# Performance work log

Hardware: AMD Instinct MI355X
Metric: run time of the kernel (lower is better)

The kernel has to match this reference:

```python
import jax, jax.numpy as jnp
import numpy as np

B, N, C, H = 2, 2048, 1024, 16
D = C // H
SCALE = D ** -0.5


def setup_inputs() -> dict:
    key = jax.random.key(0)
    ks = jax.random.split(key, 5)
    x = jax.random.normal(ks[0], (B, N, C), dtype=jnp.float32)
    # causal mask, broadcast over batch: True = attend
    attention_mask = jnp.broadcast_to(jnp.tril(jnp.ones((N, N), dtype=bool)), (B, N, N))
    w_qkv = jax.random.normal(ks[1], (3 * C, C), dtype=jnp.float32) * (C ** -0.5)
    b_qkv = jax.random.normal(ks[2], (3 * C,), dtype=jnp.float32) * 0.02
    w_proj = jax.random.normal(ks[3], (C, C), dtype=jnp.float32) * (C ** -0.5)
    b_proj = jax.random.normal(ks[4], (C,), dtype=jnp.float32) * 0.02
    return {"x": x, "attention_mask": attention_mask, "w_qkv": w_qkv,
            "b_qkv": b_qkv, "w_proj": w_proj, "b_proj": b_proj}


def reference(x, attention_mask, w_qkv, b_qkv, w_proj, b_proj):
    b, n, c = x.shape
    qkv = x @ w_qkv.T + b_qkv                      # [B,N,3C]
    qkv = qkv.reshape(b, n, 3, H, D).transpose(2, 0, 3, 1, 4)  # [3,B,H,N,D]
    q, k, v = qkv[0], qkv[1], qkv[2]
    dots = jnp.einsum('bhid,bhjd->bhij', q, k) * SCALE
    mask_value = -jnp.finfo(dots.dtype).max
    dots = jnp.where(attention_mask[:, None, :, :], dots, mask_value)
    attn = jax.nn.softmax(dots.astype(jnp.float32), axis=-1).astype(dots.dtype)
    out = jnp.einsum('bhij,bhjd->bhid', attn, v)   # [B,H,N,D]
    # NOTE: original code reshapes WITHOUT transposing heads back - faithful.
    out = out.reshape(b, n, c)
    return out @ w_proj.T + b_proj
```

## Files before the change

### kernel.cpp

```cpp
#include <hip/hip_runtime.h>
#include <hip/hip_bf16.h>
#include <stdint.h>

#define SL_F 0.18033688011112043f

typedef unsigned short u16;
typedef unsigned int u32;
typedef __attribute__((ext_vector_type(8))) short bf16x8;
typedef __attribute__((ext_vector_type(4))) float f32x4;

__device__ __forceinline__ u16 f2bf(float f) {
    union { float f; u32 u; } v; v.f = f;
    return (u16)((v.u + 0x7fffu + ((v.u >> 16) & 1u)) >> 16);
}
__device__ __forceinline__ u32 pack2bf(float a, float b) {
    union { __hip_bfloat162 h; u32 u; } p;
    p.h = __float22bfloat162_rn(make_float2(a, b));
    return p.u;
}

__device__ __forceinline__ void gl_lds16(const u16* g, u16* l) {
    __builtin_amdgcn_global_load_lds(
        (const __attribute__((address_space(1))) u32*)g,
        (__attribute__((address_space(3))) u32*)l, 16, 0, 0);
}

__global__ __launch_bounds__(256) void convert_k(
    const float* __restrict__ x, const float* __restrict__ w1,
    const float* __restrict__ w2,
    u16* __restrict__ xb, u16* __restrict__ w1b, u16* __restrict__ w2b)
{
    const int t = blockIdx.x * 256 + threadIdx.x;
    const int XA = 524288, XW1 = 393216;
    const float* src; u16* dst; int s;
    if (t < XA)            { src = x;  dst = xb;  s = t; }
    else if (t < XA + XW1) { src = w1; dst = w1b; s = t - XA; }
    else                   { src = w2; dst = w2b; s = t - XA - XW1; }
    const int c = s >> 6;
    const int u = s & 63;
    const int l = (u >> 2) + 16 * (u & 3);
    const int g = c >> 5, kb = c & 31;
    const int row = g * 16 + (l & 15);
    const int k0 = kb * 32 + (l >> 4) * 8;
    const float4 v0 = *(const float4*)&src[(size_t)row * 1024 + k0];
    const float4 v1 = *(const float4*)&src[(size_t)row * 1024 + k0 + 4];
    uint4 o;
    o.x = pack2bf(v0.x, v0.y); o.y = pack2bf(v0.z, v0.w);
    o.z = pack2bf(v1.x, v1.y); o.w = pack2bf(v1.z, v1.w);
    *(uint4*)&dst[((size_t)c * 64 + l) * 8] = o;
}

__global__ __launch_bounds__(256) void qkv_gemm(
    const u16* __restrict__ A, const u16* __restrict__ Bw,
    const float* __restrict__ bias,
    u16* __restrict__ Qb, u16* __restrict__ Kb, u16* __restrict__ VTb)
{
    __shared__ __align__(16) u16 Al[2][8 * 512];
    __shared__ __align__(16) u16 Bl[2][8 * 512];
    const int tid = threadIdx.x;
    const int lane = tid & 63;
    const int w = tid >> 6;
    const int la = lane & 15, qd = lane >> 4;
    const int m0 = blockIdx.y * 128;
    const int n0 = blockIdx.x * 128;
    const int wm = (w >> 1) * 64, wn = (w & 1) * 64;

    const u16* Ag0 = A + ((size_t)((m0 >> 4) + 2 * w) * 32) * 512 + lane * 8;
    const u16* Ag1 = Ag0 + 32 * 512;
    const u16* Bg0 = Bw + ((size_t)((n0 >> 4) + 2 * w) * 32) * 512 + lane * 8;
    const u16* Bg1 = Bg0 + 32 * 512;

    auto stage = [&](int k0, int b) {
        const size_t ko = (size_t)(k0 >> 5) * 512;
        gl_lds16(Ag0 + ko, &Al[b][(2 * w) * 512]);
        gl_lds16(Ag1 + ko, &Al[b][(2 * w + 1) * 512]);
        gl_lds16(Bg0 + ko, &Bl[b][(2 * w) * 512]);
        gl_lds16(Bg1 + ko, &Bl[b][(2 * w + 1) * 512]);
    };

    f32x4 acc[4][4] = {};
    int buf = 0;
    stage(0, 0);

    for (int k0 = 0; k0 < 1024; k0 += 32) {
        __syncthreads();
        if (k0 + 32 < 1024) stage(k0 + 32, buf ^ 1);

        bf16x8 af[4], bfr[4];
#pragma unroll
        for (int i = 0; i < 4; i++)
            af[i] = *(const bf16x8*)&Al[buf][(((unsigned)wm >> 4) + i) * 512 + lane * 8];
#pragma unroll
        for (int j = 0; j < 4; j++)
            bfr[j] = *(const bf16x8*)&Bl[buf][(((unsigned)wn >> 4) + j) * 512 + lane * 8];
#pragma unroll
        for (int i = 0; i < 4; i++)
#pragma unroll
            for (int j = 0; j < 4; j++)
                acc[i][j] = __builtin_amdgcn_mfma_f32_16x16x32_bf16(
                    af[i], bfr[j], acc[i][j], 0, 0, 0);
        buf ^= 1;
    }

    const int b_ = m0 >> 11;
    const int nb = (m0 & 2047) + wm;
#pragma unroll
    for (int j = 0; j < 4; j++) {
        const int colb = n0 + wn + j * 16;
        const int col = colb + la;
        const float bv = bias[col];
        const int t = colb >> 10;
        const int hd = col & 1023, h = hd >> 6, d = hd & 63;
        const int bh = b_ * 16 + h;
        if (t == 0) {
            u16* QB = Qb + ((size_t)bh * 2048 + nb) * 64 + d;
#pragma unroll
            for (int i = 0; i < 4; i++)
#pragma unroll
                for (int r = 0; r < 4; r++)
                    QB[(i * 16 + qd * 4 + r) * 64] =
                        f2bf((acc[i][j][r] + bv) * SL_F);
        } else if (t == 1) {
            u16* KB = Kb + (size_t)bh * 131072
                    + (size_t)((nb >> 4) * 2 + (d >> 5)) * 512 + (d & 31);
#pragma unroll
            for (int i = 0; i < 4; i++)
#pragma unroll
                for (int r = 0; r < 4; r++)
                    KB[i * 1024 + (qd * 4 + r) * 32] = f2bf(acc[i][j][r] + bv);
        } else {
            u16* VB = VTb + (size_t)bh * 131072
                    + (size_t)(d >> 4) * 32768 + (d & 15) * 32;
#pragma unroll
            for (int i = 0; i < 4; i++)
#pragma unroll
                for (int r = 0; r < 4; r++)
                    VB[((nb >> 5) + (i >> 1)) * 512 + (i & 1) * 16 + qd * 4 + r]
                        = f2bf(acc[i][j][r] + bv);
        }
    }
}

__global__ __launch_bounds__(256) void proj_gemm(
    const u16* __restrict__ A, const u16* __restrict__ Bw,
    const float* __restrict__ bias, float* __restrict__ Out)
{
    __shared__ __align__(16) u16 Al[2][16 * 512];
    __shared__ __align__(16) u16 Bl[2][8 * 512];
    const int tid = threadIdx.x;
    const int lane = tid & 63;
    const int w = tid >> 6;
    const int la = lane & 15, qd = lane >> 4;
    const int K = 1024;
    const int m0 = blockIdx.y * 128;
    const int n0 = blockIdx.x * 64;
    const int wm = (w >> 1) * 64, wn = (w & 1) * 32;

    const u16* Ab[4];
#pragma unroll
    for (int t = 0; t < 4; t++) {
        const int ck = 4 * w + t, g = ck >> 1, h = ck & 1;
        Ab[t] = A + (((size_t)(m0 >> 4) + g) * 32 + h) * 512 + lane * 8;
    }
    const u16* Bg = Bw + ((size_t)((n0 >> 4) + w) * 32) * 512 + lane * 8;

    auto stage = [&](int k0, int b) {
#pragma unroll
        for (int t = 0; t < 4; t++)
            gl_lds16(Ab[t] + (size_t)(k0 >> 5) * 512, &Al[b][(4 * w + t) * 512]);
#pragma unroll
        for (int t = 0; t < 2; t++)
            gl_lds16(Bg + (size_t)((k0 >> 5) + t) * 512, &Bl[b][(2 * w + t) * 512]);
    };

    f32x4 acc[4][2] = {};
    int buf = 0;
    stage(0, 0);

    for (int k0 = 0; k0 < K; k0 += 64) {
        __syncthreads();
        if (k0 + 64 < K) stage(k0 + 64, buf ^ 1);

        bf16x8 af[4][2], bfr[2][2];
#pragma unroll
        for (int i = 0; i < 4; i++) {
            const int g = ((unsigned)wm >> 4) + i;
#pragma unroll
            for (int h = 0; h < 2; h++)
                af[i][h] = *(const bf16x8*)&Al[buf][(g * 2 + h) * 512 + lane * 8];
        }
#pragma unroll
        for (int j = 0; j < 2; j++) {
            const int g = ((unsigned)wn >> 4) + j;
#pragma unroll
            for (int h = 0; h < 2; h++)
                bfr[j][h] = *(const bf16x8*)&Bl[buf][(g * 2 + h) * 512 + lane * 8];
        }
#pragma unroll
        for (int i = 0; i < 4; i++)
#pragma unroll
            for (int j = 0; j < 2; j++) {
                f32x4 c = acc[i][j];
                c = __builtin_amdgcn_mfma_f32_16x16x32_bf16(af[i][0], bfr[j][0], c, 0, 0, 0);
                c = __builtin_amdgcn_mfma_f32_16x16x32_bf16(af[i][1], bfr[j][1], c, 0, 0, 0);
                acc[i][j] = c;
            }
        buf ^= 1;
    }

#pragma unroll
    for (int j = 0; j < 2; j++) {
        const int col = n0 + wn + j * 16 + la;
        const float bv = bias[col];
#pragma unroll
        for (int i = 0; i < 4; i++)
#pragma unroll
            for (int r = 0; r < 4; r++) {
                const int row = m0 + wm + i * 16 + qd * 4 + r;
                Out[(size_t)row * 1024 + col] = acc[i][j][r] + bv;
            }
    }
}

__global__ __launch_bounds__(512) void attn_k(
    const u16* __restrict__ Qb, const u16* __restrict__ Kb,
    const u16* __restrict__ VTb, u16* __restrict__ Ob)
{
    __shared__ __align__(16) u16 Kl[2][16 * 512];
    __shared__ __align__(16) u16 Vl[2][16 * 512];
    __shared__ __align__(16) u16 Pl[8][16 * 72];
    const int bh = blockIdx.x & 31;
    const int pairT = blockIdx.x >> 5;
    const int tid = threadIdx.x;
    const int lane = tid & 63;
    const int w = tid >> 6;
    const int la = lane & 15, qd = lane >> 4;

    const int perm = (lane & 15) * 32 + (lane >> 4) * 8;
    const u16* Kbh = Kb + (size_t)bh * 131072 + perm;
    const u16* Vbh = VTb + (size_t)bh * 131072 + perm;
    u16* Pw = &Pl[w][0];

    auto stage = [&](int j0, int b) {
#pragma unroll
        for (int t = 0; t < 2; t++) {
            const int ck = 2 * w + t;
            gl_lds16(Kbh + (size_t)((j0 >> 3) + ck) * 512, &Kl[b][ck * 512]);
            gl_lds16(Vbh + (size_t)((ck >> 2) * 64 + (j0 >> 5) + (ck & 3)) * 512,
                     &Vl[b][ck * 512]);
        }
    };

    int buf = 0;
    stage(0, 0);

    for (int half = 0; half < 2; half++) {
        const int tile = (half == 0) ? pairT : 15 - pairT;
        const int q0 = tile * 128 + w * 16;
        const int jmax = tile * 128;
        const int qrow = q0 + la;

        const u16* Qp = Qb + ((size_t)bh * 2048 + q0 + la) * 64 + qd * 8;
        const bf16x8 qf0 = *(const bf16x8*)Qp;
        const bf16x8 qf1 = *(const bf16x8*)(Qp + 32);

        f32x4 o[4] = {};
        float lsum = 0.f;

        for (int j0 = 0; j0 <= jmax; j0 += 128) {
            __syncthreads();

            const int nj = (j0 + 128 <= jmax) ? (j0 + 128) : ((half == 0) ? 0 : -1);
            if (nj >= 0) stage(nj, buf ^ 1);

            f32x4 s[8];
#pragma unroll
            for (int c = 0; c < 8; c++) {
                f32x4 z = {};
                const bf16x8 kf0 = *(const bf16x8*)&Kl[buf][(c * 2 + 0) * 512 + lane * 8];
                const bf16x8 kf1 = *(const bf16x8*)&Kl[buf][(c * 2 + 1) * 512 + lane * 8];
                z = __builtin_amdgcn_mfma_f32_16x16x32_bf16(kf0, qf0, z, 0, 0, 0);
                z = __builtin_amdgcn_mfma_f32_16x16x32_bf16(kf1, qf1, z, 0, 0, 0);
                s[c] = z;
            }

            if (j0 == jmax) {
#pragma unroll
                for (int c = 0; c < 8; c++)
#pragma unroll
                    for (int r = 0; r < 4; r++) {
                        const int j = j0 + c * 16 + qd * 4 + r;
                        float v = s[c][r];
                        v = (j > qrow) ? -1e30f : v;
                        s[c][r] = __builtin_amdgcn_exp2f(v);
                    }
            } else {
#pragma unroll
                for (int c = 0; c < 8; c++)
#pragma unroll
                    for (int r = 0; r < 4; r++)
                        s[c][r] = __builtin_amdgcn_exp2f(s[c][r]);
            }
#pragma unroll
            for (int c = 0; c < 8; c++)
#pragma unroll
                for (int r = 0; r < 4; r++)
                    lsum += s[c][r];

#pragma unroll
            for (int hh = 0; hh < 2; hh++) {
#pragma unroll
                for (int c = 0; c < 4; c++) {
                    uint2 pw;
                    pw.x = pack2bf(s[hh * 4 + c][0], s[hh * 4 + c][1]);
                    pw.y = pack2bf(s[hh * 4 + c][2], s[hh * 4 + c][3]);
                    *(uint2*)&Pw[la * 72 + c * 16 + qd * 4] = pw;
                }
                const bf16x8 pf0 = *(const bf16x8*)&Pw[la * 72 + qd * 8];
                const bf16x8 pf1 = *(const bf16x8*)&Pw[la * 72 + 32 + qd * 8];
#pragma unroll
                for (int c2 = 0; c2 < 4; c2++) {
                    const bf16x8 vf0 = *(const bf16x8*)&Vl[buf][(c2 * 4 + hh * 2 + 0) * 512 + lane * 8];
                    const bf16x8 vf1 = *(const bf16x8*)&Vl[buf][(c2 * 4 + hh * 2 + 1) * 512 + lane * 8];
                    o[c2] = __builtin_amdgcn_mfma_f32_16x16x32_bf16(pf0, vf0, o[c2], 0, 0, 0);
                    o[c2] = __builtin_amdgcn_mfma_f32_16x16x32_bf16(pf1, vf1, o[c2], 0, 0, 0);
                }
            }
            buf ^= 1;
        }

        lsum += __shfl_xor(lsum, 16, 64);
        lsum += __shfl_xor(lsum, 32, 64);
        float rinv[4];
#pragma unroll
        for (int r = 0; r < 4; r++)
            rinv[r] = 1.0f / __shfl(lsum, qd * 4 + r, 64);

        const int m = bh * 128 + (q0 >> 4);
        u16* Ot = Ob + ((size_t)(m >> 4) * 32) * 512;
        const int mm = m & 15;
#pragma unroll
        for (int c2 = 0; c2 < 4; c2++)
#pragma unroll
            for (int r = 0; r < 4; r++) {
                const int kk5 = (qd * 4 + r) * 2 + (c2 >> 1);
                const int s3 = (c2 * 2 + (la >> 3)) & 3;
                Ot[(size_t)kk5 * 512 + (mm + 16 * s3) * 8 + (la & 7)] =
                    f2bf(o[c2][r] * rinv[r]);
            }
    }
}

extern "C" void kernel_launch(void* const* d_in, const int* in_sizes, int n_in,
                              void* d_out, int out_size, void* d_ws, size_t ws_size,
                              hipStream_t stream)
{
    const float* x     = (const float*)d_in[0];
    const float* wqkv  = (const float*)d_in[2];
    const float* bqkv  = (const float*)d_in[3];
    const float* wproj = (const float*)d_in[4];
    const float* bproj = (const float*)d_in[5];
    float* out = (float*)d_out;

    u16* ws     = (u16*)d_ws;
    u16* xb     = ws;
    u16* wqkvb  = xb + 4096 * 1024;
    u16* wprojb = wqkvb + 3072 * 1024;
    u16* Qb     = wprojb + 1024 * 1024;
    u16* Kb     = Qb + 32 * 2048 * 64;
    u16* VTb    = Kb + 32 * 2048 * 64;
    u16* Ob     = VTb + 32 * 2048 * 64;

    convert_k<<<dim3(4096), dim3(256), 0, stream>>>(
        x, wqkv, wproj, xb, wqkvb, wprojb);

    qkv_gemm<<<dim3(24, 32), dim3(256), 0, stream>>>(
        xb, wqkvb, bqkv, Qb, Kb, VTb);

    attn_k<<<dim3(256), dim3(512), 0, stream>>>(Qb, Kb, VTb, Ob);

    proj_gemm<<<dim3(16, 32), dim3(256), 0, stream>>>(
        Ob, wprojb, bproj, out);
}
```

Baseline: 188.4 us.

## Process two 16-row query tiles per wave in attention, halving block size

Each wave in the attention kernel now handles 32 query rows as two 16-row sub-tiles, with 4 waves per block instead of 8. Each K and V fragment read from LDS feeds two MFMAs, which halves LDS read traffic per unit of compute. Each wave also issues twice the staging loads. The cost is roughly double the accumulator and score registers per wave, with launch_bounds(256,1), and only 4 waves per block to hide latency.

```diff
diff --git a/kernel.cpp b/kernel.cpp
--- a/kernel.cpp
+++ b/kernel.cpp
@@ -222,13 +222,13 @@
     }
 }
 
-__global__ __launch_bounds__(512) void attn_k(
+__global__ __launch_bounds__(256, 1) void attn_k(
     const u16* __restrict__ Qb, const u16* __restrict__ Kb,
     const u16* __restrict__ VTb, u16* __restrict__ Ob)
 {
     __shared__ __align__(16) u16 Kl[2][16 * 512];
     __shared__ __align__(16) u16 Vl[2][16 * 512];
-    __shared__ __align__(16) u16 Pl[8][16 * 72];
+    __shared__ __align__(16) u16 Pl[4][2][16 * 72];
     const int bh = blockIdx.x & 31;
     const int pairT = blockIdx.x >> 5;
     const int tid = threadIdx.x;
@@ -239,12 +239,13 @@
     const int perm = (lane & 15) * 32 + (lane >> 4) * 8;
     const u16* Kbh = Kb + (size_t)bh * 131072 + perm;
     const u16* Vbh = VTb + (size_t)bh * 131072 + perm;
-    u16* Pw = &Pl[w][0];
+    u16* PwA = &Pl[w][0][0];
+    u16* PwB = &Pl[w][1][0];
 
     auto stage = [&](int j0, int b) {
 #pragma unroll
-        for (int t = 0; t < 2; t++) {
-            const int ck = 2 * w + t;
+        for (int t = 0; t < 4; t++) {
+            const int ck = 4 * w + t;
             gl_lds16(Kbh + (size_t)((j0 >> 3) + ck) * 512, &Kl[b][ck * 512]);
             gl_lds16(Vbh + (size_t)((ck >> 2) * 64 + (j0 >> 5) + (ck & 3)) * 512,
                      &Vl[b][ck * 512]);
@@ -256,16 +257,19 @@
 
     for (int half = 0; half < 2; half++) {
         const int tile = (half == 0) ? pairT : 15 - pairT;
-        const int q0 = tile * 128 + w * 16;
+        const int q0 = tile * 128 + w * 32;
         const int jmax = tile * 128;
-        const int qrow = q0 + la;
+        const int qrowA = q0 + la;
+        const int qrowB = q0 + 16 + la;
 
         const u16* Qp = Qb + ((size_t)bh * 2048 + q0 + la) * 64 + qd * 8;
-        const bf16x8 qf0 = *(const bf16x8*)Qp;
-        const bf16x8 qf1 = *(const bf16x8*)(Qp + 32);
-
-        f32x4 o[4] = {};
-        float lsum = 0.f;
+        const bf16x8 qfA0 = *(const bf16x8*)Qp;
+        const bf16x8 qfA1 = *(const bf16x8*)(Qp + 32);
+        const bf16x8 qfB0 = *(const bf16x8*)(Qp + 16 * 64);
+        const bf16x8 qfB1 = *(const bf16x8*)(Qp + 16 * 64 + 32);
+
+        f32x4 oA[4] = {}, oB[4] = {};
+        float lsumA = 0.f, lsumB = 0.f;
 
         for (int j0 = 0; j0 <= jmax; j0 += 128) {
             __syncthreads();
@@ -273,15 +277,17 @@
             const int nj = (j0 + 128 <= jmax) ? (j0 + 128) : ((half == 0) ? 0 : -1);
             if (nj >= 0) stage(nj, buf ^ 1);
 
-            f32x4 s[8];
+            f32x4 sA[8], sB[8];
 #pragma unroll
             for (int c = 0; c < 8; c++) {
-                f32x4 z = {};
                 const bf16x8 kf0 = *(const bf16x8*)&Kl[buf][(c * 2 + 0) * 512 + lane * 8];
                 const bf16x8 kf1 = *(const bf16x8*)&Kl[buf][(c * 2 + 1) * 512 + lane * 8];
-                z = __builtin_amdgcn_mfma_f32_16x16x32_bf16(kf0, qf0, z, 0, 0, 0);
-                z = __builtin_amdgcn_mfma_f32_16x16x32_bf16(kf1, qf1, z, 0, 0, 0);
-                s[c] = z;
+                f32x4 zA = {}, zB = {};
+                zA = __builtin_amdgcn_mfma_f32_16x16x32_bf16(kf0, qfA0, zA, 0, 0, 0);
+                zA = __builtin_amdgcn_mfma_f32_16x16x32_bf16(kf1, qfA1, zA, 0, 0, 0);
+                zB = __builtin_amdgcn_mfma_f32_16x16x32_bf16(kf0, qfB0, zB, 0, 0, 0);
+                zB = __builtin_amdgcn_mfma_f32_16x16x32_bf16(kf1, qfB1, zB, 0, 0, 0);
+                sA[c] = zA; sB[c] = zB;
             }
 
             if (j0 == jmax) {
@@ -290,63 +296,81 @@
 #pragma unroll
                     for (int r = 0; r < 4; r++) {
                         const int j = j0 + c * 16 + qd * 4 + r;
-                        float v = s[c][r];
-                        v = (j > qrow) ? -1e30f : v;
-                        s[c][r] = __builtin_amdgcn_exp2f(v);
+                        float vA = sA[c][r], vB = sB[c][r];
+                        vA = (j > qrowA) ? -1e30f : vA;
+                        vB = (j > qrowB) ? -1e30f : vB;
+                        sA[c][r] = __builtin_amdgcn_exp2f(vA);
+                        sB[c][r] = __builtin_amdgcn_exp2f(vB);
                     }
             } else {
 #pragma unroll
                 for (int c = 0; c < 8; c++)
 #pragma unroll
-                    for (int r = 0; r < 4; r++)
-                        s[c][r] = __builtin_amdgcn_exp2f(s[c][r]);
+                    for (int r = 0; r < 4; r++) {
+                        sA[c][r] = __builtin_amdgcn_exp2f(sA[c][r]);
+                        sB[c][r] = __builtin_amdgcn_exp2f(sB[c][r]);
+                    }
             }
 #pragma unroll
             for (int c = 0; c < 8; c++)
 #pragma unroll
-                for (int r = 0; r < 4; r++)
-                    lsum += s[c][r];
+                for (int r = 0; r < 4; r++) {
+                    lsumA += sA[c][r];
+                    lsumB += sB[c][r];
+                }
 
 #pragma unroll
             for (int hh = 0; hh < 2; hh++) {
 #pragma unroll
                 for (int c = 0; c < 4; c++) {
-                    uint2 pw;
-                    pw.x = pack2bf(s[hh * 4 + c][0], s[hh * 4 + c][1]);
-                    pw.y = pack2bf(s[hh * 4 + c][2], s[hh * 4 + c][3]);
-                    *(uint2*)&Pw[la * 72 + c * 16 + qd * 4] = pw;
+                    uint2 pwA, pwB;
+                    pwA.x = pack2bf(sA[hh * 4 + c][0], sA[hh * 4 + c][1]);
+                    pwA.y = pack2bf(sA[hh * 4 + c][2], sA[hh * 4 + c][3]);
+                    pwB.x = pack2bf(sB[hh * 4 + c][0], sB[hh * 4 + c][1]);
+                    pwB.y = pack2bf(sB[hh * 4 + c][2], sB[hh * 4 + c][3]);
+                    *(uint2*)&PwA[la * 72 + c * 16 + qd * 4] = pwA;
+                    *(uint2*)&PwB[la * 72 + c * 16 + qd * 4] = pwB;
                 }
-                const bf16x8 pf0 = *(const bf16x8*)&Pw[la * 72 + qd * 8];
-                const bf16x8 pf1 = *(const bf16x8*)&Pw[la * 72 + 32 + qd * 8];
+                const bf16x8 pfA0 = *(const bf16x8*)&PwA[la * 72 + qd * 8];
+                const bf16x8 pfA1 = *(const bf16x8*)&PwA[la * 72 + 32 + qd * 8];
+                const bf16x8 pfB0 = *(const bf16x8*)&PwB[la * 72 + qd * 8];
+                const bf16x8 pfB1 = *(const bf16x8*)&PwB[la * 72 + 32 + qd * 8];
 #pragma unroll
                 for (int c2 = 0; c2 < 4; c2++) {
                     const bf16x8 vf0 = *(const bf16x8*)&Vl[buf][(c2 * 4 + hh * 2 + 0) * 512 + lane * 8];
                     const bf16x8 vf1 = *(const bf16x8*)&Vl[buf][(c2 * 4 + hh * 2 + 1) * 512 + lane * 8];
-                    o[c2] = __builtin_amdgcn_mfma_f32_16x16x32_bf16(pf0, vf0, o[c2], 0, 0, 0);
-                    o[c2] = __builtin_amdgcn_mfma_f32_16x16x32_bf16(pf1, vf1, o[c2], 0, 0, 0);
+                    oA[c2] = __builtin_amdgcn_mfma_f32_16x16x32_bf16(pfA0, vf0, oA[c2], 0, 0, 0);
+                    oA[c2] = __builtin_amdgcn_mfma_f32_16x16x32_bf16(pfA1, vf1, oA[c2], 0, 0, 0);
+                    oB[c2] = __builtin_amdgcn_mfma_f32_16x16x32_bf16(pfB0, vf0, oB[c2], 0, 0, 0);
+                    oB[c2] = __builtin_amdgcn_mfma_f32_16x16x32_bf16(pfB1, vf1, oB[c2], 0, 0, 0);
                 }
             }
             buf ^= 1;
         }
 
-        lsum += __shfl_xor(lsum, 16, 64);
-        lsum += __shfl_xor(lsum, 32, 64);
-        float rinv[4];
-#pragma unroll
-        for (int r = 0; r < 4; r++)
-            rinv[r] = 1.0f / __shfl(lsum, qd * 4 + r, 64);
+        lsumA += __shfl_xor(lsumA, 16, 64);
+        lsumA += __shfl_xor(lsumA, 32, 64);
+        lsumB += __shfl_xor(lsumB, 16, 64);
+        lsumB += __shfl_xor(lsumB, 32, 64);
+        float rinvA[4], rinvB[4];
+#pragma unroll
+        for (int r = 0; r < 4; r++) {
+            rinvA[r] = 1.0f / __shfl(lsumA, qd * 4 + r, 64);
+            rinvB[r] = 1.0f / __shfl(lsumB, qd * 4 + r, 64);
+        }
 
         const int m = bh * 128 + (q0 >> 4);
+        const int mm = m & 15;
         u16* Ot = Ob + ((size_t)(m >> 4) * 32) * 512;
-        const int mm = m & 15;
 #pragma unroll
         for (int c2 = 0; c2 < 4; c2++)
 #pragma unroll
             for (int r = 0; r < 4; r++) {
                 const int kk5 = (qd * 4 + r) * 2 + (c2 >> 1);
                 const int s3 = (c2 * 2 + (la >> 3)) & 3;
-                Ot[(size_t)kk5 * 512 + (mm + 16 * s3) * 8 + (la & 7)] =
-                    f2bf(o[c2][r] * rinv[r]);
+                const size_t base = (size_t)kk5 * 512 + 16 * s3 * 8 + (la & 7);
+                Ot[base + mm * 8]       = f2bf(oA[c2][r] * rinvA[r]);
+                Ot[base + (mm + 1) * 8] = f2bf(oB[c2][r] * rinvB[r]);
             }
     }
 }
@@ -377,7 +401,7 @@
     qkv_gemm<<<dim3(24, 32), dim3(256), 0, stream>>>(
         xb, wqkvb, bqkv, Qb, Kb, VTb);
 
-    attn_k<<<dim3(256), dim3(512), 0, stream>>>(Qb, Kb, VTb, Ob);
+    attn_k<<<dim3(256), dim3(256), 0, stream>>>(Qb, Kb, VTb, Ob);
 
     proj_gemm<<<dim3(16, 32), dim3(256), 0, stream>>>(
         Ob, wprojb, bproj, out);
```

Result: slower. 195.2 us (+3.6%).

## Stage 256-key chunks per barrier and raise wave priority around MFMAs

Applied to the files above, without the earlier changes.

The attention kernel now stages two 128-key tiles of K and V into LDS per double-buffer step, halving the number of block barriers and async load rounds per query tile. Each step processes two sub-tiles and skips the second when it lies beyond the causal diagonal. It also wraps the QK and PV MFMA loops in s_setprio so matrix work gets issue priority over other waves. LDS use doubles, to roughly 140KB for K/V plus P, which may limit occupancy, and the odd-tile tail stages data that is never used.

```diff
diff --git a/kernel.cpp b/kernel.cpp
--- a/kernel.cpp
+++ b/kernel.cpp
@@ -226,8 +226,8 @@
     const u16* __restrict__ Qb, const u16* __restrict__ Kb,
     const u16* __restrict__ VTb, u16* __restrict__ Ob)
 {
-    __shared__ __align__(16) u16 Kl[2][16 * 512];
-    __shared__ __align__(16) u16 Vl[2][16 * 512];
+    __shared__ __align__(16) u16 Kl[2][32 * 512];
+    __shared__ __align__(16) u16 Vl[2][32 * 512];
     __shared__ __align__(16) u16 Pl[8][16 * 72];
     const int bh = blockIdx.x & 31;
     const int pairT = blockIdx.x >> 5;
@@ -241,12 +241,12 @@
     const u16* Vbh = VTb + (size_t)bh * 131072 + perm;
     u16* Pw = &Pl[w][0];
 
-    auto stage = [&](int j0, int b) {
-#pragma unroll
-        for (int t = 0; t < 2; t++) {
-            const int ck = 2 * w + t;
-            gl_lds16(Kbh + (size_t)((j0 >> 3) + ck) * 512, &Kl[b][ck * 512]);
-            gl_lds16(Vbh + (size_t)((ck >> 2) * 64 + (j0 >> 5) + (ck & 3)) * 512,
+    auto stage = [&](int jj, int b) {
+#pragma unroll
+        for (int t = 0; t < 4; t++) {
+            const int ck = 4 * w + t;
+            gl_lds16(Kbh + (size_t)(jj * 16 + ck) * 512, &Kl[b][ck * 512]);
+            gl_lds16(Vbh + (size_t)((ck >> 3) * 64 + jj * 4 + (ck & 7)) * 512,
                      &Vl[b][ck * 512]);
         }
     };
@@ -257,8 +257,8 @@
     for (int half = 0; half < 2; half++) {
         const int tile = (half == 0) ? pairT : 15 - pairT;
         const int q0 = tile * 128 + w * 16;
-        const int jmax = tile * 128;
         const int qrow = q0 + la;
+        const int S = (tile + 2) >> 1;
 
         const u16* Qp = Qb + ((size_t)bh * 2048 + q0 + la) * 64 + qd * 8;
         const bf16x8 qf0 = *(const bf16x8*)Qp;
@@ -267,63 +267,75 @@
         f32x4 o[4] = {};
         float lsum = 0.f;
 
-        for (int j0 = 0; j0 <= jmax; j0 += 128) {
+        for (int st = 0; st < S; ++st) {
+            const int jj = 2 * st;
             __syncthreads();
 
-            const int nj = (j0 + 128 <= jmax) ? (j0 + 128) : ((half == 0) ? 0 : -1);
+            const int nj = (st + 1 < S) ? (jj + 2) : ((half == 0) ? 0 : -1);
             if (nj >= 0) stage(nj, buf ^ 1);
 
-            f32x4 s[8];
-#pragma unroll
-            for (int c = 0; c < 8; c++) {
-                f32x4 z = {};
-                const bf16x8 kf0 = *(const bf16x8*)&Kl[buf][(c * 2 + 0) * 512 + lane * 8];
-                const bf16x8 kf1 = *(const bf16x8*)&Kl[buf][(c * 2 + 1) * 512 + lane * 8];
-                z = __builtin_amdgcn_mfma_f32_16x16x32_bf16(kf0, qf0, z, 0, 0, 0);
-                z = __builtin_amdgcn_mfma_f32_16x16x32_bf16(kf1, qf1, z, 0, 0, 0);
-                s[c] = z;
-            }
-
-            if (j0 == jmax) {
+#pragma unroll
+            for (int sub = 0; sub < 2; ++sub) {
+                const int jjj = jj + sub;
+                if (jjj > tile) continue;
+                const int koff = sub * 16;
+
+                f32x4 s[8];
+                __builtin_amdgcn_s_setprio(1);
+#pragma unroll
+                for (int c = 0; c < 8; c++) {
+                    f32x4 z = {};
+                    const bf16x8 kf0 = *(const bf16x8*)&Kl[buf][(koff + c * 2 + 0) * 512 + lane * 8];
+                    const bf16x8 kf1 = *(const bf16x8*)&Kl[buf][(koff + c * 2 + 1) * 512 + lane * 8];
+                    z = __builtin_amdgcn_mfma_f32_16x16x32_bf16(kf0, qf0, z, 0, 0, 0);
+                    z = __builtin_amdgcn_mfma_f32_16x16x32_bf16(kf1, qf1, z, 0, 0, 0);
+                    s[c] = z;
+                }
+                __builtin_amdgcn_s_setprio(0);
+
+                if (jjj == tile) {
+#pragma unroll
+                    for (int c = 0; c < 8; c++)
+#pragma unroll
+                        for (int r = 0; r < 4; r++) {
+                            const int j = jjj * 128 + c * 16 + qd * 4 + r;
+                            float v = s[c][r];
+                            v = (j > qrow) ? -1e30f : v;
+                            s[c][r] = __builtin_amdgcn_exp2f(v);
+                        }
+                } else {
+#pragma unroll
+                    for (int c = 0; c < 8; c++)
+#pragma unroll
+                        for (int r = 0; r < 4; r++)
+                            s[c][r] = __builtin_amdgcn_exp2f(s[c][r]);
+                }
 #pragma unroll
                 for (int c = 0; c < 8; c++)
 #pragma unroll
-                    for (int r = 0; r < 4; r++) {
-                        const int j = j0 + c * 16 + qd * 4 + r;
-                        float v = s[c][r];
-                        v = (j > qrow) ? -1e30f : v;
-                        s[c][r] = __builtin_amdgcn_exp2f(v);
+                    for (int r = 0; r < 4; r++)
+                        lsum += s[c][r];
+
+#pragma unroll
+                for (int hh = 0; hh < 2; hh++) {
+#pragma unroll
+                    for (int c = 0; c < 4; c++) {
+                        uint2 pw;
+                        pw.x = pack2bf(s[hh * 4 + c][0], s[hh * 4 + c][1]);
+                        pw.y = pack2bf(s[hh * 4 + c][2], s[hh * 4 + c][3]);
+                        *(uint2*)&Pw[la * 72 + c * 16 + qd * 4] = pw;
                     }
-            } else {
-#pragma unroll
-                for (int c = 0; c < 8; c++)
-#pragma unroll
-                    for (int r = 0; r < 4; r++)
-                        s[c][r] = __builtin_amdgcn_exp2f(s[c][r]);
-            }
-#pragma unroll
-            for (int c = 0; c < 8; c++)
-#pragma unroll
-                for (int r = 0; r < 4; r++)
-                    lsum += s[c][r];
-
-#pragma unroll
-            for (int hh = 0; hh < 2; hh++) {
-#pragma unroll
-                for (int c = 0; c < 4; c++) {
-                    uint2 pw;
-                    pw.x = pack2bf(s[hh * 4 + c][0], s[hh * 4 + c][1]);
-                    pw.y = pack2bf(s[hh * 4 + c][2], s[hh * 4 + c][3]);
-                    *(uint2*)&Pw[la * 72 + c * 16 + qd * 4] = pw;
-                }
-                const bf16x8 pf0 = *(const bf16x8*)&Pw[la * 72 + qd * 8];
-                const bf16x8 pf1 = *(const bf16x8*)&Pw[la * 72 + 32 + qd * 8];
-#pragma unroll
-                for (int c2 = 0; c2 < 4; c2++) {
-                    const bf16x8 vf0 = *(const bf16x8*)&Vl[buf][(c2 * 4 + hh * 2 + 0) * 512 + lane * 8];
-                    const bf16x8 vf1 = *(const bf16x8*)&Vl[buf][(c2 * 4 + hh * 2 + 1) * 512 + lane * 8];
-                    o[c2] = __builtin_amdgcn_mfma_f32_16x16x32_bf16(pf0, vf0, o[c2], 0, 0, 0);
-                    o[c2] = __builtin_amdgcn_mfma_f32_16x16x32_bf16(pf1, vf1, o[c2], 0, 0, 0);
+                    const bf16x8 pf0 = *(const bf16x8*)&Pw[la * 72 + qd * 8];
+                    const bf16x8 pf1 = *(const bf16x8*)&Pw[la * 72 + 32 + qd * 8];
+                    __builtin_amdgcn_s_setprio(1);
+#pragma unroll
+                    for (int c2 = 0; c2 < 4; c2++) {
+                        const bf16x8 vf0 = *(const bf16x8*)&Vl[buf][(c2 * 8 + sub * 4 + hh * 2 + 0) * 512 + lane * 8];
+                        const bf16x8 vf1 = *(const bf16x8*)&Vl[buf][(c2 * 8 + sub * 4 + hh * 2 + 1) * 512 + lane * 8];
+                        o[c2] = __builtin_amdgcn_mfma_f32_16x16x32_bf16(pf0, vf0, o[c2], 0, 0, 0);
+                        o[c2] = __builtin_amdgcn_mfma_f32_16x16x32_bf16(pf1, vf1, o[c2], 0, 0, 0);
+                    }
+                    __builtin_amdgcn_s_setprio(0);
                 }
             }
             buf ^= 1;
```

New measurement: 188.6 us. Within noise of the previous version (+0.1%).

## Split attention into one q-tile per block with 64-key tiles and causal skip

Applied to the files above, without the earlier changes.

The attention kernel stops pairing two query tiles per block and launches 512 blocks, each owning one 128-row query tile, with a reordered tile mapping. Key/value tiles shrink from 128 to 64 keys, halving the LDS buffers. A launch bound of 4 blocks per CU is added, waves skip fully masked key tiles, and s_setprio is raised around the MFMA sections. The aim is more occupancy and finer causal work skipping, at the cost of more blocks, more barriers per key and uneven per-block work.

```diff
diff --git a/kernel.cpp b/kernel.cpp
--- a/kernel.cpp
+++ b/kernel.cpp
@@ -222,15 +222,16 @@
     }
 }
 
-__global__ __launch_bounds__(512) void attn_k(
+__global__ __launch_bounds__(512, 4) void attn_k(
     const u16* __restrict__ Qb, const u16* __restrict__ Kb,
     const u16* __restrict__ VTb, u16* __restrict__ Ob)
 {
-    __shared__ __align__(16) u16 Kl[2][16 * 512];
-    __shared__ __align__(16) u16 Vl[2][16 * 512];
+    __shared__ __align__(16) u16 Kl[2][8 * 512];
+    __shared__ __align__(16) u16 Vl[2][8 * 512];
     __shared__ __align__(16) u16 Pl[8][16 * 72];
     const int bh = blockIdx.x & 31;
-    const int pairT = blockIdx.x >> 5;
+    const int s = (blockIdx.x >> 5) & 15;
+    const int T = (s < 8) ? s : 23 - s;
     const int tid = threadIdx.x;
     const int lane = tid & 63;
     const int w = tid >> 6;
@@ -241,114 +242,116 @@
     const u16* Vbh = VTb + (size_t)bh * 131072 + perm;
     u16* Pw = &Pl[w][0];
 
-    auto stage = [&](int j0, int b) {
+    auto stage = [&](int jt, int b) {
 #pragma unroll
         for (int t = 0; t < 2; t++) {
             const int ck = 2 * w + t;
-            gl_lds16(Kbh + (size_t)((j0 >> 3) + ck) * 512, &Kl[b][ck * 512]);
-            gl_lds16(Vbh + (size_t)((ck >> 2) * 64 + (j0 >> 5) + (ck & 3)) * 512,
-                     &Vl[b][ck * 512]);
+            if (ck < 8) {
+                gl_lds16(Kbh + (size_t)(jt * 8 + ck) * 512, &Kl[b][ck * 512]);
+            } else {
+                const int cv = ck - 8;
+                gl_lds16(Vbh + (size_t)((cv >> 1) * 64 + jt * 2 + (cv & 1)) * 512,
+                         &Vl[b][cv * 512]);
+            }
         }
     };
+
+    const int q0 = T * 128 + w * 16;
+    const int qrow = q0 + la;
+    const int JT = 2 * T + 2;
+
+    const u16* Qp = Qb + ((size_t)bh * 2048 + q0 + la) * 64 + qd * 8;
+    const bf16x8 qf0 = *(const bf16x8*)Qp;
+    const bf16x8 qf1 = *(const bf16x8*)(Qp + 32);
+
+    f32x4 o[4] = {};
+    float lsum = 0.f;
 
     int buf = 0;
     stage(0, 0);
 
-    for (int half = 0; half < 2; half++) {
-        const int tile = (half == 0) ? pairT : 15 - pairT;
-        const int q0 = tile * 128 + w * 16;
-        const int jmax = tile * 128;
-        const int qrow = q0 + la;
-
-        const u16* Qp = Qb + ((size_t)bh * 2048 + q0 + la) * 64 + qd * 8;
-        const bf16x8 qf0 = *(const bf16x8*)Qp;
-        const bf16x8 qf1 = *(const bf16x8*)(Qp + 32);
-
-        f32x4 o[4] = {};
-        float lsum = 0.f;
-
-        for (int j0 = 0; j0 <= jmax; j0 += 128) {
-            __syncthreads();
-
-            const int nj = (j0 + 128 <= jmax) ? (j0 + 128) : ((half == 0) ? 0 : -1);
-            if (nj >= 0) stage(nj, buf ^ 1);
-
-            f32x4 s[8];
-#pragma unroll
-            for (int c = 0; c < 8; c++) {
+    for (int jt = 0; jt < JT; ++jt) {
+        __syncthreads();
+        if (jt + 1 < JT) stage(jt + 1, buf ^ 1);
+
+        if (jt * 64 <= q0 + 15) {
+            f32x4 sv[4];
+            __builtin_amdgcn_s_setprio(1);
+#pragma unroll
+            for (int c = 0; c < 4; c++) {
                 f32x4 z = {};
                 const bf16x8 kf0 = *(const bf16x8*)&Kl[buf][(c * 2 + 0) * 512 + lane * 8];
                 const bf16x8 kf1 = *(const bf16x8*)&Kl[buf][(c * 2 + 1) * 512 + lane * 8];
                 z = __builtin_amdgcn_mfma_f32_16x16x32_bf16(kf0, qf0, z, 0, 0, 0);
                 z = __builtin_amdgcn_mfma_f32_16x16x32_bf16(kf1, qf1, z, 0, 0, 0);
-                s[c] = z;
-            }
-
-            if (j0 == jmax) {
-#pragma unroll
-                for (int c = 0; c < 8; c++)
+                sv[c] = z;
+            }
+            __builtin_amdgcn_s_setprio(0);
+
+            if (jt * 64 + 63 > q0) {
+#pragma unroll
+                for (int c = 0; c < 4; c++)
 #pragma unroll
                     for (int r = 0; r < 4; r++) {
-                        const int j = j0 + c * 16 + qd * 4 + r;
-                        float v = s[c][r];
+                        const int j = jt * 64 + c * 16 + qd * 4 + r;
+                        float v = sv[c][r];
                         v = (j > qrow) ? -1e30f : v;
-                        s[c][r] = __builtin_amdgcn_exp2f(v);
+                        sv[c][r] = __builtin_amdgcn_exp2f(v);
                     }
             } else {
 #pragma unroll
-                for (int c = 0; c < 8; c++)
+                for (int c = 0; c < 4; c++)
 #pragma unroll
                     for (int r = 0; r < 4; r++)
-                        s[c][r] = __builtin_amdgcn_exp2f(s[c][r]);
-            }
-#pragma unroll
-            for (int c = 0; c < 8; c++)
+                        sv[c][r] = __builtin_amdgcn_exp2f(sv[c][r]);
+            }
+#pragma unroll
+            for (int c = 0; c < 4; c++)
 #pragma unroll
                 for (int r = 0; r < 4; r++)
-                    lsum += s[c][r];
-
+                    lsum += sv[c][r];
+
+#pragma unroll
+            for (int c = 0; c < 4; c++) {
+                uint2 pw;
+                pw.x = pack2bf(sv[c][0], sv[c][1]);
+                pw.y = pack2bf(sv[c][2], sv[c][3]);
+                *(uint2*)&Pw[la * 72 + c * 16 + qd * 4] = pw;
+            }
 #pragma unroll
             for (int hh = 0; hh < 2; hh++) {
-#pragma unroll
-                for (int c = 0; c < 4; c++) {
-                    uint2 pw;
-                    pw.x = pack2bf(s[hh * 4 + c][0], s[hh * 4 + c][1]);
-                    pw.y = pack2bf(s[hh * 4 + c][2], s[hh * 4 + c][3]);
-                    *(uint2*)&Pw[la * 72 + c * 16 + qd * 4] = pw;
+                const bf16x8 pf = *(const bf16x8*)&Pw[la * 72 + hh * 32 + qd * 8];
+                __builtin_amdgcn_s_setprio(1);
+#pragma unroll
+                for (int c2 = 0; c2 < 4; c2++) {
+                    const bf16x8 vf = *(const bf16x8*)&Vl[buf][(c2 * 2 + hh) * 512 + lane * 8];
+                    o[c2] = __builtin_amdgcn_mfma_f32_16x16x32_bf16(pf, vf, o[c2], 0, 0, 0);
                 }
-                const bf16x8 pf0 = *(const bf16x8*)&Pw[la * 72 + qd * 8];
-                const bf16x8 pf1 = *(const bf16x8*)&Pw[la * 72 + 32 + qd * 8];
-#pragma unroll
-                for (int c2 = 0; c2 < 4; c2++) {
-                    const bf16x8 vf0 = *(const bf16x8*)&Vl[buf][(c2 * 4 + hh * 2 + 0) * 512 + lane * 8];
-                    const bf16x8 vf1 = *(const bf16x8*)&Vl[buf][(c2 * 4 + hh * 2 + 1) * 512 + lane * 8];
-                    o[c2] = __builtin_amdgcn_mfma_f32_16x16x32_bf16(pf0, vf0, o[c2], 0, 0, 0);
-                    o[c2] = __builtin_amdgcn_mfma_f32_16x16x32_bf16(pf1, vf1, o[c2], 0, 0, 0);
-                }
-            }
-            buf ^= 1;
-        }
-
-        lsum += __shfl_xor(lsum, 16, 64);
-        lsum += __shfl_xor(lsum, 32, 64);
-        float rinv[4];
-#pragma unroll
-        for (int r = 0; r < 4; r++)
-            rinv[r] = 1.0f / __shfl(lsum, qd * 4 + r, 64);
-
-        const int m = bh * 128 + (q0 >> 4);
-        u16* Ot = Ob + ((size_t)(m >> 4) * 32) * 512;
-        const int mm = m & 15;
-#pragma unroll
-        for (int c2 = 0; c2 < 4; c2++)
-#pragma unroll
-            for (int r = 0; r < 4; r++) {
-                const int kk5 = (qd * 4 + r) * 2 + (c2 >> 1);
-                const int s3 = (c2 * 2 + (la >> 3)) & 3;
-                Ot[(size_t)kk5 * 512 + (mm + 16 * s3) * 8 + (la & 7)] =
-                    f2bf(o[c2][r] * rinv[r]);
-            }
-    }
+                __builtin_amdgcn_s_setprio(0);
+            }
+        }
+        buf ^= 1;
+    }
+
+    lsum += __shfl_xor(lsum, 16, 64);
+    lsum += __shfl_xor(lsum, 32, 64);
+    float rinv[4];
+#pragma unroll
+    for (int r = 0; r < 4; r++)
+        rinv[r] = 1.0f / __shfl(lsum, qd * 4 + r, 64);
+
+    const int m = bh * 128 + (q0 >> 4);
+    u16* Ot = Ob + ((size_t)(m >> 4) * 32) * 512;
+    const int mm = m & 15;
+#pragma unroll
+    for (int c2 = 0; c2 < 4; c2++)
+#pragma unroll
+        for (int r = 0; r < 4; r++) {
+            const int kk5 = (qd * 4 + r) * 2 + (c2 >> 1);
+            const int s3 = (c2 * 2 + (la >> 3)) & 3;
+            Ot[(size_t)kk5 * 512 + (mm + 16 * s3) * 8 + (la & 7)] =
+                f2bf(o[c2][r] * rinv[r]);
+        }
 }
 
 extern "C" void kernel_launch(void* const* d_in, const int* in_sizes, int n_in,
@@ -377,7 +380,7 @@
     qkv_gemm<<<dim3(24, 32), dim3(256), 0, stream>>>(
         xb, wqkvb, bqkv, Qb, Kb, VTb);
 
-    attn_k<<<dim3(256), dim3(512), 0, stream>>>(Qb, Kb, VTb, Ob);
+    attn_k<<<dim3(512), dim3(512), 0, stream>>>(Qb, Kb, VTb, Ob);
 
     proj_gemm<<<dim3(16, 32), dim3(256), 0, stream>>>(
         Ob, wprojb, bproj, out);
```

After: 187.4 us. No clear change (-0.6%).
